# Performance work log

Hardware: AMD Instinct MI355X
Metric: run time of the kernel (lower is better)

The kernel has to match this reference:

```python
import jax, jax.numpy as jnp
import numpy as np

B, T, F, M = 32, 256, 512, 4   # batch, pred_len (=d_model=state_size), feature_dim (=mamba seq), time-mark feats
N = F - M                      # number of variates in x_enc
T2 = 2 * T
EPS = 1e-5


def setup_inputs() -> dict:
    key = jax.random.key(0)
    it = iter(jax.random.split(key, 32))
    def nrm(*s):
        return jax.random.normal(next(it), s, jnp.float32) * 0.02
    inp = {
        "x_enc": jax.random.normal(next(it), (B, T, N), jnp.float32),
        "x_mark_enc": jax.random.normal(next(it), (B, T, M), jnp.float32),
        "x_dec": jnp.zeros((1, 1, 1), jnp.float32),
        "x_mark_dec": jnp.zeros((1, 1, 1), jnp.float32),
        # 3 structurally identical MambaBlocks -> stack params on leading dim 3
        "norm_w": jnp.ones((3, T), jnp.float32),
        "inp_W": nrm(3, T, T2), "inp_b": jnp.zeros((3, T2), jnp.float32),
        "conv_W": nrm(3, F, F, 3), "conv_b": jnp.zeros((3, F), jnp.float32),
        "convlin_W": nrm(3, T2, T2), "convlin_b": jnp.zeros((3, T2), jnp.float32),
        "fc1_W": nrm(3, T2, T2), "fc1_b": jnp.zeros((3, T2), jnp.float32),
        "fc2_W": nrm(3, T2, T), "fc2_b": jnp.zeros((3, T), jnp.float32),
        "fc3_W": nrm(3, T2, T), "fc3_b": jnp.zeros((3, T), jnp.float32),
        "D_W": nrm(3, T, T2), "D_b": jnp.zeros((3, T2), jnp.float32),
        "out_W": nrm(3, T2, T), "out_b": jnp.ones((3, T), jnp.float32),  # out_proj.bias init to 1.0
        "proj_W": nrm(T, T), "proj_b": jnp.zeros((T,), jnp.float32),
    }
    return inp


def _rmsnorm(x, w):
    return x * jax.lax.rsqrt(jnp.mean(x * x, -1, keepdims=True) + EPS) * w


def _conv1d(x, W, b):
    # x: [B, C, L], W: [C_out, C_in, 3], padding=1
    y = jax.lax.conv_general_dilated(x, W, (1,), [(1, 1)], dimension_numbers=("NCH", "OIH", "NCH"))
    return y + b[None, :, None]


def _s6(x, fc1W, fc1b, fc2W, fc2b, fc3W, fc3b):
    # h is zero-initialized each call, so dA=exp(delta*A) multiplies zeros and
    # y = einsum('bln,bldn->bld', C, x[...,None]*dB) = delta * x * <C,B>_n
    Bmat = x @ fc2W + fc2b                         # [B, L, n]
    Cmat = x @ fc3W + fc3b                         # [B, L, n]
    delta = jax.nn.softplus(x @ fc1W + fc1b)       # [B, L, d]
    cb = jnp.einsum("bln,bln->bl", Cmat, Bmat)   # contraction over state dim
    return delta * x * cb[:, :, None]


def _block(x, i, p):
    xn = _rmsnorm(x, p["norm_w"][i])
    xp = xn @ p["inp_W"][i] + p["inp_b"][i]                      # [B, F, 2T]
    xc = jax.nn.silu(_conv1d(xp, p["conv_W"][i], p["conv_b"][i]))
    xco = xc @ p["convlin_W"][i] + p["convlin_b"][i]
    xssm = _s6(xco, p["fc1_W"][i], p["fc1_b"][i], p["fc2_W"][i], p["fc2_b"][i], p["fc3_W"][i], p["fc3_b"][i])
    xres = jax.nn.silu(xn @ p["D_W"][i] + p["D_b"][i])
    return (jax.nn.silu(xssm) * xres) @ p["out_W"][i] + p["out_b"][i]


def _forward(x_enc, x_mark_enc, p):
    means = jax.lax.stop_gradient(jnp.mean(x_enc, 1, keepdims=True))  # detached in torch
    xe = x_enc - means
    stdev = jnp.sqrt(jnp.var(xe, axis=1, keepdims=True) + 1e-5)       # NOT detached in torch
    xe = xe / stdev
    x = jnp.concatenate([xe, x_mark_enc], axis=2).transpose(0, 2, 1)  # [B, F, T]
    for i in range(3):
        x = _block(x, i, p)
    dec = (x @ p["proj_W"] + p["proj_b"]).transpose(0, 2, 1)          # [B, T, F]
    return dec[:, :, :N] * stdev + means                              # pred_len == T


def reference(x_enc, x_mark_enc, x_dec, x_mark_dec, norm_w, inp_W, inp_b, conv_W, conv_b, convlin_W, convlin_b, fc1_W, fc1_b, fc2_W, fc2_b, fc3_W, fc3_b, D_W, D_b, out_W, out_b, proj_W, proj_b):
    p = dict(norm_w=norm_w, inp_W=inp_W, inp_b=inp_b, conv_W=conv_W, conv_b=conv_b, convlin_W=convlin_W, convlin_b=convlin_b, fc1_W=fc1_W, fc1_b=fc1_b, fc2_W=fc2_W, fc2_b=fc2_b, fc3_W=fc3_W, fc3_b=fc3_b, D_W=D_W, D_b=D_b, out_W=out_W, out_b=out_b, proj_W=proj_W, proj_b=proj_b)
    return _forward(x_enc, x_mark_enc, p)
```

## Files before the change

### kernel.cpp

```cpp
#include <hip/hip_runtime.h>
#include <hip/hip_bf16.h>
#include <math.h>

typedef __hip_bfloat16 bf16;
typedef short short8 __attribute__((ext_vector_type(8)));
typedef short short4v __attribute__((ext_vector_type(4)));
typedef float floatx4 __attribute__((ext_vector_type(4)));

constexpr int CB_ = 32;
constexpr int CT = 256;
constexpr int CF = 512;
constexpr int CN = 508;
constexpr int CM = 4;
constexpr int CT2 = 512;
constexpr int MROWS = CB_ * CF;
constexpr int PADL = 528;

__device__ __forceinline__ float b2f(bf16 v) { return __bfloat162float(v); }
__device__ __forceinline__ bf16 f2b(float v) { return __float2bfloat16(v); }
__device__ __forceinline__ float s2f(short s) {
    unsigned u = ((unsigned)(unsigned short)s) << 16;
    return __builtin_bit_cast(float, u);
}
__device__ __forceinline__ short f2s(float v) {
    bf16 t = __float2bfloat16(v);
    return __builtin_bit_cast(short, t);
}
__device__ __forceinline__ float silu_f(float x) { return x / (1.0f + __expf(-x)); }
__device__ __forceinline__ float softplus_f(float x) {
    return fmaxf(x, 0.0f) + __logf(1.0f + __expf(-fabsf(x)));
}

__device__ __forceinline__ void gl_lds16(const bf16* g, short* l) {
    __builtin_amdgcn_global_load_lds(
        (const __attribute__((address_space(1))) unsigned int*)(g),
        (__attribute__((address_space(3))) unsigned int*)(l), 16, 0, 0);
}

constexpr int CONVN = 3 * 3 * 512 * 512;
constexpr int MTILES = 3520;
struct P8 { const float* s[8]; bf16* d[8]; };
__global__ __launch_bounds__(256) void prepack_all_kernel(P8 p, const float* __restrict__ nw,
                                                          const float* __restrict__ convW,
                                                          bf16* __restrict__ convD,
                                                          bf16* __restrict__ xpT,
                                                          float* __restrict__ CBv) {
    int bid = blockIdx.x;
    if (bid >= MTILES) {
        int idx = (bid - MTILES) * 256 + threadIdx.x;
        if (idx < CONVN) {
            int ci = idx & 511;
            int co = (idx >> 9) & 511;
            int it = idx >> 18;
            int tap = it % 3, ib = it / 3;
            convD[idx] = f2b(convW[(((size_t)(ib * 512 + co)) * 512 + ci) * 3 + tap]);
        } else if (idx < CONVN + 32768) {
            int j = idx - CONVN;
            int ci = j & 511;
            int w = (j >> 9) & 1;
            int b = j >> 10;
            xpT[((size_t)b * PADL + (w ? 513 : 0)) * 512 + ci] = f2b(0.0f);
        } else if (idx < CONVN + 32768 + MROWS) {
            CBv[idx - CONVN - 32768] = 0.0f;
        }
        return;
    }
    const int Ks[8]   = {256, 256, 512, 512, 512, 512, 512, 256};
    const int Ns[8]   = {512, 512, 512, 256, 256, 512, 256, 256};
    const int zs[8]   = {3, 3, 3, 3, 3, 3, 3, 1};
    const int dstr[8] = {262144, 262144, 524288, 524288, 524288, 262144, 131072, 65536};
    const int rml[8]  = {1, 1, 1, 2, 2, 1, 1, 1};
    const int rad[8]  = {0, 0, 0, 0, 1, 0, 0, 0};
    int m = 0, acc = 0;
    for (m = 0; m < 8; m++) {
        int c = (Ns[m] >> 5) * (Ks[m] >> 5) * zs[m];
        if (bid < acc + c) break;
        acc += c;
    }
    int lid = bid - acc;
    int K = Ks[m], N = Ns[m];
    int tx = N >> 5, ty = K >> 5;
    int z = lid / (tx * ty), rem = lid % (tx * ty);
    int k0 = (rem / tx) * 32, n0 = (rem % tx) * 32;
    const float* s = p.s[m] + (size_t)z * K * N;
    bf16* d = p.d[m] + (size_t)z * dstr[m];
    int mul = rml[m], add = rad[m];
    bool fold = (m <= 1);
    __shared__ float Ts[32][33];
    for (int e = threadIdx.x; e < 1024; e += 256) {
        int r = e >> 5, c = e & 31;
        float v = s[(size_t)(k0 + r) * N + n0 + c];
        if (fold) v *= nw[z * 256 + k0 + r];
        Ts[r][c] = v;
    }
    __syncthreads();
    for (int e = threadIdx.x; e < 1024; e += 256) {
        int r = e >> 5, c = e & 31;
        d[(size_t)((n0 + r) * mul + add) * K + k0 + c] = f2b(Ts[c][r]);
    }
}

__global__ __launch_bounds__(256) void buildx_kernel(
    const float* __restrict__ xe, const float* __restrict__ xm,
    float* __restrict__ means, float* __restrict__ stdev,
    bf16* __restrict__ X0, float* __restrict__ SCL) {
    __shared__ float L[256][65];
    __shared__ float red_s[4][64], red_q[4][64];
    __shared__ float stat_m[64], stat_i[64];
    int blk = blockIdx.x;
    int b = blk >> 3, f0 = (blk & 7) * 64;
    int tid = threadIdx.x;
    int j = tid & 63, tq = tid >> 6;
    int f = f0 + j;
    float ps = 0.f, pq = 0.f;
    const float* xep = xe + (size_t)b * CT * CN + f;
    const float* xmp = xm + (size_t)b * CT * CM + (f - CN);
    #pragma unroll 4
    for (int tt = 0; tt < 64; tt++) {
        int t = tq * 64 + tt;
        float v = (f < CN) ? xep[(size_t)t * CN] : xmp[(size_t)t * CM];
        L[t][j] = v;
        ps += v;
        pq += v * v;
    }
    red_s[tq][j] = ps;
    red_q[tq][j] = pq;
    __syncthreads();
    if (tid < 64) {
        int ff = f0 + tid;
        float s = red_s[0][tid] + red_s[1][tid] + red_s[2][tid] + red_s[3][tid];
        float q = red_q[0][tid] + red_q[1][tid] + red_q[2][tid] + red_q[3][tid];
        float mean, isd, msq;
        if (ff < CN) {
            mean = s * (1.0f / 256.0f);
            float var = fmaxf(q * (1.0f / 256.0f) - mean * mean, 0.0f);
            float sd = sqrtf(var + 1e-5f);
            isd = 1.0f / sd;
            means[b * CN + ff] = mean;
            stdev[b * CN + ff] = sd;
            msq = var / (var + 1e-5f);
        } else {
            mean = 0.0f;
            isd = 1.0f;
            msq = q * (1.0f / 256.0f);
        }
        stat_m[tid] = mean;
        stat_i[tid] = isd;
        SCL[b * 512 + ff] = rsqrtf(msq + 1e-5f);
    }
    __syncthreads();
    bf16* outp = X0 + ((size_t)(b * 512 + f0)) * 256;
    int t = tid;
    #pragma unroll 4
    for (int fp = 0; fp < 64; fp++) {
        float val = (L[t][fp] - stat_m[fp]) * stat_i[fp];
        outp[(size_t)fp * 256 + t] = f2b(val);
    }
}

template <int MODE>
__global__ __launch_bounds__(256) void mgemm_kernel(const bf16* __restrict__ A,
                                                    const bf16* __restrict__ Wt,
                                                    const float* __restrict__ b1,
                                                    const float* __restrict__ b2,
                                                    const float* __restrict__ SCL,
                                                    bf16* __restrict__ o1,
                                                    bf16* __restrict__ o2,
                                                    int K, int Ncols) {
    __shared__ __align__(16) short As[128 * 32];
    __shared__ __align__(16) short Bs[128 * 32];
    const int tid = threadIdx.x;
    const int lane = tid & 63;
    const int wave = tid >> 6;
    const int m0 = blockIdx.x * 128, n0 = blockIdx.y * 128;

    const int srow0 = wave * 32;
    const int lrow = lane >> 2;
    const int lcol = (lane & 3) * 8;

    const bf16* aP0 = A + (size_t)(m0 + srow0 + lrow) * K + lcol;
    const bf16* aP1 = A + (size_t)(m0 + srow0 + 16 + lrow) * K + lcol;
    const bf16* bP0 = Wt + (size_t)(n0 + srow0 + lrow) * K + lcol;
    const bf16* bP1 = Wt + (size_t)(n0 + srow0 + 16 + lrow) * K + lcol;
    short* aL0 = &As[srow0 * 32];
    short* aL1 = &As[(srow0 + 16) * 32];
    short* bL0 = &Bs[srow0 * 32];
    short* bL1 = &Bs[(srow0 + 16) * 32];

    const int wm = (wave & 1) * 64, wn = (wave >> 1) * 64;
    const int fr = lane & 15, quad = lane >> 4;

    floatx4 acc[4][4];
    #pragma unroll
    for (int i = 0; i < 4; i++)
        #pragma unroll
        for (int j = 0; j < 4; j++) acc[i][j] = (floatx4){0.f, 0.f, 0.f, 0.f};

    for (int k0 = 0; k0 < K; k0 += 32) {
        gl_lds16(aP0 + k0, aL0);
        gl_lds16(aP1 + k0, aL1);
        gl_lds16(bP0 + k0, bL0);
        gl_lds16(bP1 + k0, bL1);
        __syncthreads();
        short8 af[4], bfv[4];
        #pragma unroll
        for (int i = 0; i < 4; i++) af[i] = *(const short8*)&As[(wm + i * 16 + fr) * 32 + quad * 8];
        #pragma unroll
        for (int j = 0; j < 4; j++) bfv[j] = *(const short8*)&Bs[(wn + j * 16 + fr) * 32 + quad * 8];
        #pragma unroll
        for (int i = 0; i < 4; i++)
            #pragma unroll
            for (int j = 0; j < 4; j++)
                acc[i][j] = __builtin_amdgcn_mfma_f32_16x16x32_bf16(af[i], bfv[j], acc[i][j], 0, 0, 0);
        __syncthreads();
    }

    if (MODE == 0) {
        #pragma unroll
        for (int j = 0; j < 4; j++) {
            int n = n0 + wn + j * 16 + fr;
            float bv = b1[n];
            #pragma unroll
            for (int i = 0; i < 4; i++) {
                int mb = m0 + wm + i * 16 + quad * 4;
                #pragma unroll
                for (int r = 0; r < 4; r++)
                    o1[(size_t)(mb + r) * Ncols + n] = f2b(acc[i][j][r] + bv);
            }
        }
    } else {
        if (n0 + wn < 512) {
            int b = (m0 + wm) >> 9;
            #pragma unroll
            for (int i = 0; i < 4; i++) {
                int mb = m0 + wm + i * 16 + quad * 4;
                float sclr[4];
                #pragma unroll
                for (int r = 0; r < 4; r++) sclr[r] = SCL[mb + r];
                #pragma unroll
                for (int j = 0; j < 4; j++) {
                    int n = n0 + wn + j * 16 + fr;
                    float bv = b1[n];
                    bf16* dst = o1 + ((size_t)b * PADL + n + 1) * 512;
                    int ci = mb & 511;
                    short4v pk;
                    #pragma unroll
                    for (int r = 0; r < 4; r++) pk[r] = f2s(acc[i][j][r] * sclr[r] + bv);
                    *(short4v*)(dst + ci) = pk;
                }
            }
        } else {
            #pragma unroll
            for (int i = 0; i < 4; i++) {
                int mb = m0 + wm + i * 16 + quad * 4;
                float sclr[4];
                #pragma unroll
                for (int r = 0; r < 4; r++) sclr[r] = SCL[mb + r];
                #pragma unroll
                for (int j = 0; j < 4; j++) {
                    int n = n0 + wn + j * 16 + fr;
                    float bv = b2[n - 512];
                    #pragma unroll
                    for (int r = 0; r < 4; r++)
                        o2[(size_t)(mb + r) * 512 + (n - 512)] =
                            f2b(silu_f(acc[i][j][r] * sclr[r] + bv));
                }
            }
        }
    }
}

__global__ __launch_bounds__(256) void cbgemm_kernel(const bf16* __restrict__ A,
                                                     const bf16* __restrict__ Wt,
                                                     const float* __restrict__ b2,
                                                     const float* __restrict__ b3,
                                                     float* __restrict__ CBv) {
    __shared__ __align__(16) short As[128 * 32];
    __shared__ __align__(16) short Bs[128 * 32];
    const int tid = threadIdx.x;
    const int lane = tid & 63;
    const int wave = tid >> 6;
    const int m0 = blockIdx.x * 128, n0 = blockIdx.y * 128;

    const int srow0 = wave * 32;
    const int lrow = lane >> 2;
    const int lcol = (lane & 3) * 8;
    const bf16* aP0 = A + (size_t)(m0 + srow0 + lrow) * 512 + lcol;
    const bf16* aP1 = A + (size_t)(m0 + srow0 + 16 + lrow) * 512 + lcol;
    const bf16* bP0 = Wt + (size_t)(n0 + srow0 + lrow) * 512 + lcol;
    const bf16* bP1 = Wt + (size_t)(n0 + srow0 + 16 + lrow) * 512 + lcol;
    short* aL0 = &As[srow0 * 32];
    short* aL1 = &As[(srow0 + 16) * 32];
    short* bL0 = &Bs[srow0 * 32];
    short* bL1 = &Bs[(srow0 + 16) * 32];

    const int wm = (wave & 1) * 64, wn = (wave >> 1) * 64;
    const int fr = lane & 15, quad = lane >> 4;

    floatx4 acc[4][4];
    #pragma unroll
    for (int i = 0; i < 4; i++)
        #pragma unroll
        for (int j = 0; j < 4; j++) acc[i][j] = (floatx4){0.f, 0.f, 0.f, 0.f};

    for (int k0 = 0; k0 < 512; k0 += 32) {
        gl_lds16(aP0 + k0, aL0);
        gl_lds16(aP1 + k0, aL1);
        gl_lds16(bP0 + k0, bL0);
        gl_lds16(bP1 + k0, bL1);
        __syncthreads();
        short8 af[4], bfv[4];
        #pragma unroll
        for (int i = 0; i < 4; i++) af[i] = *(const short8*)&As[(wm + i * 16 + fr) * 32 + quad * 8];
        #pragma unroll
        for (int j = 0; j < 4; j++) bfv[j] = *(const short8*)&Bs[(wn + j * 16 + fr) * 32 + quad * 8];
        #pragma unroll
        for (int i = 0; i < 4; i++)
            #pragma unroll
            for (int j = 0; j < 4; j++)
                acc[i][j] = __builtin_amdgcn_mfma_f32_16x16x32_bf16(af[i], bfv[j], acc[i][j], 0, 0, 0);
        __syncthreads();
    }
    int nnb = n0 + wn;
    float bv[4];
    #pragma unroll
    for (int j = 0; j < 4; j++) {
        int nn = nnb + j * 16 + fr;
        int c = nn >> 1;
        bv[j] = (fr & 1) ? b3[c] : b2[c];
    }
    #pragma unroll
    for (int i = 0; i < 4; i++) {
        #pragma unroll
        for (int r = 0; r < 4; r++) {
            float s = 0.f;
            #pragma unroll
            for (int j = 0; j < 4; j++) {
                float v = acc[i][j][r] + bv[j];
                s += v * __shfl_xor(v, 1);
            }
            s += __shfl_xor(s, 2);
            s += __shfl_xor(s, 4);
            s += __shfl_xor(s, 8);
            if (fr == 0)
                atomicAdd(&CBv[m0 + wm + i * 16 + quad * 4 + r], s * 0.5f);
        }
    }
}

__global__ __launch_bounds__(256) void fc1gate_kernel(const bf16* __restrict__ A,
                                                      const bf16* __restrict__ Wt,
                                                      const float* __restrict__ b1,
                                                      const float* __restrict__ CBv,
                                                      const bf16* __restrict__ Xres,
                                                      bf16* __restrict__ G) {
    __shared__ __align__(16) short As[128 * 32];
    __shared__ __align__(16) short Bs[128 * 32];
    const int tid = threadIdx.x;
    const int lane = tid & 63;
    const int wave = tid >> 6;
    const int m0 = blockIdx.x * 128, n0 = blockIdx.y * 128;

    const int srow0 = wave * 32;
    const int lrow = lane >> 2;
    const int lcol = (lane & 3) * 8;
    const bf16* aP0 = A + (size_t)(m0 + srow0 + lrow) * 512 + lcol;
    const bf16* aP1 = A + (size_t)(m0 + srow0 + 16 + lrow) * 512 + lcol;
    const bf16* bP0 = Wt + (size_t)(n0 + srow0 + lrow) * 512 + lcol;
    const bf16* bP1 = Wt + (size_t)(n0 + srow0 + 16 + lrow) * 512 + lcol;
    short* aL0 = &As[srow0 * 32];
    short* aL1 = &As[(srow0 + 16) * 32];
    short* bL0 = &Bs[srow0 * 32];
    short* bL1 = &Bs[(srow0 + 16) * 32];

    const int wm = (wave & 1) * 64, wn = (wave >> 1) * 64;
    const int fr = lane & 15, quad = lane >> 4;

    floatx4 acc[4][4];
    #pragma unroll
    for (int i = 0; i < 4; i++)
        #pragma unroll
        for (int j = 0; j < 4; j++) acc[i][j] = (floatx4){0.f, 0.f, 0.f, 0.f};

    for (int k0 = 0; k0 < 512; k0 += 32) {
        gl_lds16(aP0 + k0, aL0);
        gl_lds16(aP1 + k0, aL1);
        gl_lds16(bP0 + k0, bL0);
        gl_lds16(bP1 + k0, bL1);
        __syncthreads();
        short8 af[4], bfv[4];
        #pragma unroll
        for (int i = 0; i < 4; i++) af[i] = *(const short8*)&As[(wm + i * 16 + fr) * 32 + quad * 8];
        #pragma unroll
        for (int j = 0; j < 4; j++) bfv[j] = *(const short8*)&Bs[(wn + j * 16 + fr) * 32 + quad * 8];
        #pragma unroll
        for (int i = 0; i < 4; i++)
            #pragma unroll
            for (int j = 0; j < 4; j++)
                acc[i][j] = __builtin_amdgcn_mfma_f32_16x16x32_bf16(af[i], bfv[j], acc[i][j], 0, 0, 0);
        __syncthreads();
    }
    #pragma unroll
    for (int i = 0; i < 4; i++) {
        int mb = m0 + wm + i * 16 + quad * 4;
        float cbr[4];
        #pragma unroll
        for (int r = 0; r < 4; r++) cbr[r] = CBv[mb + r];
        #pragma unroll
        for (int j = 0; j < 4; j++) {
            int n = n0 + wn + j * 16 + fr;
            float bv = b1[n];
            #pragma unroll
            for (int r = 0; r < 4; r++) {
                size_t off = (size_t)(mb + r) * 512 + n;
                float delta = softplus_f(acc[i][j][r] + bv);
                float xssm = delta * b2f(A[off]) * cbr[r];
                G[off] = f2b(silu_f(xssm) * b2f(Xres[off]));
            }
        }
    }
}

__global__ __launch_bounds__(256) void conv_mfma_kernel(const bf16* __restrict__ Wc,
                                                        const bf16* __restrict__ xpT,
                                                        const float* __restrict__ bias,
                                                        bf16* __restrict__ Out,
                                                        float* __restrict__ CBvZ) {
    __shared__ __align__(16) short As[3 * 128 * 32];
    __shared__ __align__(16) short Bs[144 * 32];
    const int tid = threadIdx.x;
    const int lane = tid & 63;
    const int wave = tid >> 6;
    int bx = blockIdx.x;
    if (bx < 128 && tid < 128) CBvZ[bx * 128 + tid] = 0.0f;
    int xcd = bx & 7, g = bx >> 3;
    int mt = g & 3;
    int id = xcd * 16 + (g >> 2);
    int nt = id & 3, b = id >> 2;
    const int m0 = mt * 128, n0 = nt * 128;
    const bf16* xb = xpT + (size_t)b * PADL * 512;

    const int lrow = lane >> 2;
    const int lcol = (lane & 3) * 8;
    const int wm = (wave & 1) * 64, wn = (wave >> 1) * 64;
    const int fr = lane & 15, quad = lane >> 4;

    floatx4 acc[4][4];
    #pragma unroll
    for (int i = 0; i < 4; i++)
        #pragma unroll
        for (int j = 0; j < 4; j++) acc[i][j] = (floatx4){0.f, 0.f, 0.f, 0.f};

    for (int k0 = 0; k0 < 512; k0 += 32) {
        for (int ga = wave; ga < 24; ga += 4) {
            int tap = ga >> 3, rg = ga & 7;
            gl_lds16(Wc + (size_t)tap * 262144 + (size_t)(m0 + rg * 16 + lrow) * 512 + k0 + lcol,
                     &As[ga * 512]);
        }
        for (int gb = wave; gb < 9; gb += 4) {
            gl_lds16(xb + (size_t)(n0 + gb * 16 + lrow) * 512 + k0 + lcol, &Bs[gb * 512]);
        }
        __syncthreads();
        #pragma unroll
        for (int tap = 0; tap < 3; tap++) {
            short8 af[4], bfv[4];
            #pragma unroll
            for (int i = 0; i < 4; i++)
                af[i] = *(const short8*)&As[tap * 4096 + (wm + i * 16 + fr) * 32 + quad * 8];
            #pragma unroll
            for (int j = 0; j < 4; j++)
                bfv[j] = *(const short8*)&Bs[(wn + j * 16 + fr + tap) * 32 + quad * 8];
            #pragma unroll
            for (int i = 0; i < 4; i++)
                #pragma unroll
                for (int j = 0; j < 4; j++)
                    acc[i][j] = __builtin_amdgcn_mfma_f32_16x16x32_bf16(af[i], bfv[j], acc[i][j], 0, 0, 0);
        }
        __syncthreads();
    }
    bf16* ob = Out + (size_t)b * CF * CT2;
    #pragma unroll
    for (int i = 0; i < 4; i++) {
        int mb = m0 + wm + i * 16 + quad * 4;
        #pragma unroll
        for (int r = 0; r < 4; r++) {
            float bv = bias[mb + r];
            #pragma unroll
            for (int j = 0; j < 4; j++) {
                int n = n0 + wn + j * 16 + fr;
                ob[(size_t)(mb + r) * CT2 + n] = f2b(silu_f(acc[i][j][r] + bv));
            }
        }
    }
}

__global__ __launch_bounds__(256) void gemm_scl_kernel(const bf16* __restrict__ A,
                                                       const bf16* __restrict__ Wt,
                                                       const float* __restrict__ bias,
                                                       bf16* __restrict__ Xo,
                                                       float* __restrict__ SCL) {
    __shared__ __align__(16) short As[64 * 32];
    __shared__ __align__(16) short Bs[256 * 32];
    __shared__ float red[4][64];
    const int tid = threadIdx.x;
    const int lane = tid & 63;
    const int wave = tid >> 6;
    const int m0 = blockIdx.x * 64;

    const int lrow = lane >> 2;
    const int lcol = (lane & 3) * 8;
    const bf16* aP = A + (size_t)(m0 + wave * 16 + lrow) * 512 + lcol;
    short* aL = &As[wave * 16 * 32];
    const bf16* bP[4];
    short* bL[4];
    #pragma unroll
    for (int g = 0; g < 4; g++) {
        int r0 = (wave * 4 + g) * 16;
        bP[g] = Wt + (size_t)(r0 + lrow) * 512 + lcol;
        bL[g] = &Bs[r0 * 32];
    }
    const int wn = wave * 64;
    const int fr = lane & 15, quad = lane >> 4;

    floatx4 acc[4][4];
    #pragma unroll
    for (int i = 0; i < 4; i++)
        #pragma unroll
        for (int j = 0; j < 4; j++) acc[i][j] = (floatx4){0.f, 0.f, 0.f, 0.f};

    for (int k0 = 0; k0 < 512; k0 += 32) {
        gl_lds16(aP + k0, aL);
        #pragma unroll
        for (int g = 0; g < 4; g++) gl_lds16(bP[g] + k0, bL[g]);
        __syncthreads();
        short8 af[4], bfv[4];
        #pragma unroll
        for (int i = 0; i < 4; i++) af[i] = *(const short8*)&As[(i * 16 + fr) * 32 + quad * 8];
        #pragma unroll
        for (int j = 0; j < 4; j++) bfv[j] = *(const short8*)&Bs[(wn + j * 16 + fr) * 32 + quad * 8];
        #pragma unroll
        for (int i = 0; i < 4; i++)
            #pragma unroll
            for (int j = 0; j < 4; j++)
                acc[i][j] = __builtin_amdgcn_mfma_f32_16x16x32_bf16(af[i], bfv[j], acc[i][j], 0, 0, 0);
        __syncthreads();
    }
    #pragma unroll
    for (int j = 0; j < 4; j++) {
        float bv = bias[wn + j * 16 + fr];
        #pragma unroll
        for (int i = 0; i < 4; i++)
            #pragma unroll
            for (int r = 0; r < 4; r++) acc[i][j][r] += bv;
    }
    #pragma unroll
    for (int i = 0; i < 4; i++) {
        #pragma unroll
        for (int r = 0; r < 4; r++) {
            float s = 0.f;
            #pragma unroll
            for (int j = 0; j < 4; j++) s += acc[i][j][r] * acc[i][j][r];
            #pragma unroll
            for (int o = 8; o > 0; o >>= 1) s += __shfl_xor(s, o);
            if (fr == 0) red[wave][i * 16 + quad * 4 + r] = s;
        }
    }
    __syncthreads();
    if (tid < 64) {
        float tot = red[0][tid] + red[1][tid] + red[2][tid] + red[3][tid];
        SCL[m0 + tid] = rsqrtf(tot * (1.0f / CT) + 1e-5f);
    }
    #pragma unroll
    for (int j = 0; j < 4; j++) {
        int n = wn + j * 16 + fr;
        #pragma unroll
        for (int i = 0; i < 4; i++) {
            int rl = i * 16 + quad * 4;
            #pragma unroll
            for (int r = 0; r < 4; r++)
                Xo[(size_t)(m0 + rl + r) * CT + n] = f2b(acc[i][j][r]);
        }
    }
}

__global__ __launch_bounds__(256) void proj_out_kernel(const bf16* __restrict__ A,
                                                       const bf16* __restrict__ Wt,
                                                       const float* __restrict__ bias,
                                                       const float* __restrict__ means,
                                                       const float* __restrict__ stdev,
                                                       float* __restrict__ out) {
    __shared__ __align__(16) short As[128 * 32];
    __shared__ __align__(16) short Bs[128 * 32];
    const int tid = threadIdx.x;
    const int lane = tid & 63;
    const int wave = tid >> 6;
    const int m0 = blockIdx.x * 128, n0 = blockIdx.y * 128;

    const int srow0 = wave * 32;
    const int lrow = lane >> 2;
    const int lcol = (lane & 3) * 8;
    const bf16* aP0 = A + (size_t)(m0 + srow0 + lrow) * 256 + lcol;
    const bf16* aP1 = A + (size_t)(m0 + srow0 + 16 + lrow) * 256 + lcol;
    const bf16* bP0 = Wt + (size_t)(n0 + srow0 + lrow) * 256 + lcol;
    const bf16* bP1 = Wt + (size_t)(n0 + srow0 + 16 + lrow) * 256 + lcol;
    short* aL0 = &As[srow0 * 32];
    short* aL1 = &As[(srow0 + 16) * 32];
    short* bL0 = &Bs[srow0 * 32];
    short* bL1 = &Bs[(srow0 + 16) * 32];

    const int wm = (wave & 1) * 64, wn = (wave >> 1) * 64;
    const int fr = lane & 15, quad = lane >> 4;

    floatx4 acc[4][4];
    #pragma unroll
    for (int i = 0; i < 4; i++)
        #pragma unroll
        for (int j = 0; j < 4; j++) acc[i][j] = (floatx4){0.f, 0.f, 0.f, 0.f};

    for (int k0 = 0; k0 < 256; k0 += 32) {
        gl_lds16(aP0 + k0, aL0);
        gl_lds16(aP1 + k0, aL1);
        gl_lds16(bP0 + k0, bL0);
        gl_lds16(bP1 + k0, bL1);
        __syncthreads();
        short8 af[4], bfv[4];
        #pragma unroll
        for (int i = 0; i < 4; i++) af[i] = *(const short8*)&As[(wm + i * 16 + fr) * 32 + quad * 8];
        #pragma unroll
        for (int j = 0; j < 4; j++) bfv[j] = *(const short8*)&Bs[(wn + j * 16 + fr) * 32 + quad * 8];
        #pragma unroll
        for (int i = 0; i < 4; i++)
            #pragma unroll
            for (int j = 0; j < 4; j++)
                acc[i][j] = __builtin_amdgcn_mfma_f32_16x16x32_bf16(af[i], bfv[j], acc[i][j], 0, 0, 0);
        __syncthreads();
    }
    #pragma unroll
    for (int j = 0; j < 4; j++) {
        int t = n0 + wn + j * 16 + fr;
        float bv = bias[t];
        #pragma unroll
        for (int i = 0; i < 4; i++) {
            int mb = m0 + wm + i * 16 + quad * 4;
            int b = mb >> 9;
            int nv = mb & 511;
            if (nv < CN) {
                floatx4 o;
                #pragma unroll
                for (int r = 0; r < 4; r++) {
                    int sn = b * CN + nv + r;
                    o[r] = (acc[i][j][r] + bv) * stdev[sn] + means[sn];
                }
                *(floatx4*)(out + ((size_t)(b * CT + t)) * CN + nv) = o;
            }
        }
    }
}

extern "C" void kernel_launch(void* const* d_in, const int* in_sizes, int n_in,
                              void* d_out, int out_size, void* d_ws, size_t ws_size,
                              hipStream_t stream) {
    const float* x_enc  = (const float*)d_in[0];
    const float* x_mark = (const float*)d_in[1];
    const float* norm_w = (const float*)d_in[4];
    const float* inp_W  = (const float*)d_in[5];
    const float* inp_b  = (const float*)d_in[6];
    const float* conv_W = (const float*)d_in[7];
    const float* conv_b = (const float*)d_in[8];
    const float* convlin_W = (const float*)d_in[9];
    const float* convlin_b = (const float*)d_in[10];
    const float* fc1_W = (const float*)d_in[11];
    const float* fc1_b = (const float*)d_in[12];
    const float* fc2_W = (const float*)d_in[13];
    const float* fc2_b = (const float*)d_in[14];
    const float* fc3_W = (const float*)d_in[15];
    const float* fc3_b = (const float*)d_in[16];
    const float* D_W   = (const float*)d_in[17];
    const float* D_b   = (const float*)d_in[18];
    const float* out_W = (const float*)d_in[19];
    const float* out_b = (const float*)d_in[20];
    const float* proj_W = (const float*)d_in[21];
    const float* proj_b = (const float*)d_in[22];

    char* ws = (char*)d_ws;
    float* MEANS = (float*)(ws);
    float* STDEV = (float*)(ws + 65536);
    float* CBv   = (float*)(ws + 131072);
    float* SCL   = (float*)(ws + 196608);
    bf16* wt = (bf16*)(ws + 262144);
    bf16* wt_g1      = wt;
    bf16* wt_g3      = wt + 786432;
    bf16* wt_convlin = wt + 2359296;
    bf16* wt_out     = wt + 3145728;
    bf16* wt_proj    = wt + 3538944;
    bf16* wt_conv    = wt + 3604480;
    bf16* xpT = (bf16*)(ws + 12189696);
    const size_t POOLB = 16777216;
    bf16* pool[4] = {
        (bf16*)(ws + 29491200),
        (bf16*)(ws + 29491200 + POOLB),
        (bf16*)(ws + 29491200 + 2 * POOLB),
        (bf16*)(ws + 29491200 + 3 * POOLB),
    };
    float* out = (float*)d_out;

    P8 p;
    p.s[0] = inp_W;  p.d[0] = wt_g1;
    p.s[1] = D_W;    p.d[1] = wt_g1 + 131072;
    p.s[2] = fc1_W;  p.d[2] = wt_g3;
    p.s[3] = fc2_W;  p.d[3] = wt_g3 + 262144;
    p.s[4] = fc3_W;  p.d[4] = wt_g3 + 262144;
    p.s[5] = convlin_W; p.d[5] = wt_convlin;
    p.s[6] = out_W;  p.d[6] = wt_out;
    p.s[7] = proj_W; p.d[7] = wt_proj;
    int convBlocks = (CONVN + 32768 + MROWS + 255) / 256;
    prepack_all_kernel<<<MTILES + convBlocks, 256, 0, stream>>>(
        p, norm_w, conv_W, wt_conv, xpT, CBv);

    buildx_kernel<<<256, 256, 0, stream>>>(x_enc, x_mark, MEANS, STDEV, pool[0], SCL);

    int ia = 0, ico = 1, ires = 2, iout = 3;
    for (int i = 0; i < 3; i++) {
        bf16* A  = pool[ia];
        bf16* XCO = pool[ico];
        bf16* XRES = pool[ires];
        bf16* OUTP = pool[iout];

        mgemm_kernel<1><<<dim3(128, 8), 256, 0, stream>>>(
            A, wt_g1 + (size_t)i * 262144, inp_b + i * CT2, D_b + i * CT2, SCL,
            xpT, XRES, 256, 1024);
        conv_mfma_kernel<<<512, 256, 0, stream>>>(wt_conv + (size_t)i * 786432, xpT,
                                                  conv_b + i * CF, A, CBv);
        mgemm_kernel<0><<<dim3(128, 4), 256, 0, stream>>>(
            A, wt_convlin + (size_t)i * 262144, convlin_b + i * CT2, nullptr, nullptr,
            XCO, nullptr, 512, 512);
        cbgemm_kernel<<<dim3(128, 4), 256, 0, stream>>>(
            XCO, wt_g3 + (size_t)i * 524288 + 262144, fc2_b + i * CT, fc3_b + i * CT, CBv);
        fc1gate_kernel<<<dim3(128, 4), 256, 0, stream>>>(
            XCO, wt_g3 + (size_t)i * 524288, fc1_b + i * CT2, CBv, XRES, A);
        gemm_scl_kernel<<<256, 256, 0, stream>>>(
            A, wt_out + (size_t)i * 131072, out_b + i * CT, OUTP, SCL);

        int na = iout, nco = ia, nres = ico, nout = ires;
        ia = na; ico = nco; ires = nres; iout = nout;
    }

    proj_out_kernel<<<dim3(128, 2), 256, 0, stream>>>(
        pool[ia], wt_proj, proj_b, MEANS, STDEV, out);
}
```

Before: 558.7 us.

## Double K-tile depth to 64 with XOR-swizzled LDS layout in all GEMMs

Every MFMA GEMM kernel now stages a K-slice of 64 instead of 32 per iteration, which halves the number of barrier pairs and global-to-LDS load rounds. LDS rows are 128 bytes wide and use an XOR swizzle on the 16-byte column chunk, so the fragment reads avoid bank conflicts. The conv kernel's shifted-row reads use a swizzle that accounts for the tap offset. The cost is double the LDS footprint per block, which may lower occupancy, most of all in the conv kernel.

```diff
diff --git a/kernel.cpp b/kernel.cpp
--- a/kernel.cpp
+++ b/kernel.cpp
@@ -18,10 +18,6 @@
 
 __device__ __forceinline__ float b2f(bf16 v) { return __bfloat162float(v); }
 __device__ __forceinline__ bf16 f2b(float v) { return __float2bfloat16(v); }
-__device__ __forceinline__ float s2f(short s) {
-    unsigned u = ((unsigned)(unsigned short)s) << 16;
-    return __builtin_bit_cast(float, u);
-}
 __device__ __forceinline__ short f2s(float v) {
     bf16 t = __float2bfloat16(v);
     return __builtin_bit_cast(short, t);
@@ -36,6 +32,7 @@
         (const __attribute__((address_space(1))) unsigned int*)(g),
         (__attribute__((address_space(3))) unsigned int*)(l), 16, 0, 0);
 }
+
 
 constexpr int CONVN = 3 * 3 * 512 * 512;
 constexpr int MTILES = 3520;
@@ -167,28 +164,32 @@
                                                     bf16* __restrict__ o1,
                                                     bf16* __restrict__ o2,
                                                     int K, int Ncols) {
-    __shared__ __align__(16) short As[128 * 32];
-    __shared__ __align__(16) short Bs[128 * 32];
+    __shared__ __align__(16) short As[128 * 64];
+    __shared__ __align__(16) short Bs[128 * 64];
     const int tid = threadIdx.x;
     const int lane = tid & 63;
     const int wave = tid >> 6;
     const int m0 = blockIdx.x * 128, n0 = blockIdx.y * 128;
 
     const int srow0 = wave * 32;
-    const int lrow = lane >> 2;
-    const int lcol = (lane & 3) * 8;
-
-    const bf16* aP0 = A + (size_t)(m0 + srow0 + lrow) * K + lcol;
-    const bf16* aP1 = A + (size_t)(m0 + srow0 + 16 + lrow) * K + lcol;
-    const bf16* bP0 = Wt + (size_t)(n0 + srow0 + lrow) * K + lcol;
-    const bf16* bP1 = Wt + (size_t)(n0 + srow0 + 16 + lrow) * K + lcol;
-    short* aL0 = &As[srow0 * 32];
-    short* aL1 = &As[(srow0 + 16) * 32];
-    short* bL0 = &Bs[srow0 * 32];
-    short* bL1 = &Bs[(srow0 + 16) * 32];
+    const int lrow8 = lane >> 3;
+    const int lcolS = (((lane & 7) ^ lrow8) << 3);
+
+    const bf16* aPc[4];
+    const bf16* bPc[4];
+    short* aLc[4];
+    short* bLc[4];
+    #pragma unroll
+    for (int c = 0; c < 4; c++) {
+        aPc[c] = A + (size_t)(m0 + srow0 + c * 8 + lrow8) * K + lcolS;
+        bPc[c] = Wt + (size_t)(n0 + srow0 + c * 8 + lrow8) * K + lcolS;
+        aLc[c] = &As[(srow0 + c * 8) * 64];
+        bLc[c] = &Bs[(srow0 + c * 8) * 64];
+    }
 
     const int wm = (wave & 1) * 64, wn = (wave >> 1) * 64;
     const int fr = lane & 15, quad = lane >> 4;
+    const int fr7 = fr & 7;
 
     floatx4 acc[4][4];
     #pragma unroll
@@ -196,22 +197,27 @@
         #pragma unroll
         for (int j = 0; j < 4; j++) acc[i][j] = (floatx4){0.f, 0.f, 0.f, 0.f};
 
-    for (int k0 = 0; k0 < K; k0 += 32) {
-        gl_lds16(aP0 + k0, aL0);
-        gl_lds16(aP1 + k0, aL1);
-        gl_lds16(bP0 + k0, bL0);
-        gl_lds16(bP1 + k0, bL1);
-        __syncthreads();
-        short8 af[4], bfv[4];
-        #pragma unroll
-        for (int i = 0; i < 4; i++) af[i] = *(const short8*)&As[(wm + i * 16 + fr) * 32 + quad * 8];
-        #pragma unroll
-        for (int j = 0; j < 4; j++) bfv[j] = *(const short8*)&Bs[(wn + j * 16 + fr) * 32 + quad * 8];
-        #pragma unroll
-        for (int i = 0; i < 4; i++)
-            #pragma unroll
-            for (int j = 0; j < 4; j++)
-                acc[i][j] = __builtin_amdgcn_mfma_f32_16x16x32_bf16(af[i], bfv[j], acc[i][j], 0, 0, 0);
+    for (int k0 = 0; k0 < K; k0 += 64) {
+        #pragma unroll
+        for (int c = 0; c < 4; c++) {
+            gl_lds16(aPc[c] + k0, aLc[c]);
+            gl_lds16(bPc[c] + k0, bLc[c]);
+        }
+        __syncthreads();
+        #pragma unroll
+        for (int s = 0; s < 2; s++) {
+            const int co = (((s * 4 + quad) ^ fr7) << 3);
+            short8 af[4], bfv[4];
+            #pragma unroll
+            for (int i = 0; i < 4; i++) af[i] = *(const short8*)&As[(wm + i * 16 + fr) * 64 + co];
+            #pragma unroll
+            for (int j = 0; j < 4; j++) bfv[j] = *(const short8*)&Bs[(wn + j * 16 + fr) * 64 + co];
+            #pragma unroll
+            for (int i = 0; i < 4; i++)
+                #pragma unroll
+                for (int j = 0; j < 4; j++)
+                    acc[i][j] = __builtin_amdgcn_mfma_f32_16x16x32_bf16(af[i], bfv[j], acc[i][j], 0, 0, 0);
+        }
         __syncthreads();
     }
 
@@ -275,27 +281,31 @@
                                                      const float* __restrict__ b2,
                                                      const float* __restrict__ b3,
                                                      float* __restrict__ CBv) {
-    __shared__ __align__(16) short As[128 * 32];
-    __shared__ __align__(16) short Bs[128 * 32];
+    __shared__ __align__(16) short As[128 * 64];
+    __shared__ __align__(16) short Bs[128 * 64];
     const int tid = threadIdx.x;
     const int lane = tid & 63;
     const int wave = tid >> 6;
     const int m0 = blockIdx.x * 128, n0 = blockIdx.y * 128;
 
     const int srow0 = wave * 32;
-    const int lrow = lane >> 2;
-    const int lcol = (lane & 3) * 8;
-    const bf16* aP0 = A + (size_t)(m0 + srow0 + lrow) * 512 + lcol;
-    const bf16* aP1 = A + (size_t)(m0 + srow0 + 16 + lrow) * 512 + lcol;
-    const bf16* bP0 = Wt + (size_t)(n0 + srow0 + lrow) * 512 + lcol;
-    const bf16* bP1 = Wt + (size_t)(n0 + srow0 + 16 + lrow) * 512 + lcol;
-    short* aL0 = &As[srow0 * 32];
-    short* aL1 = &As[(srow0 + 16) * 32];
-    short* bL0 = &Bs[srow0 * 32];
-    short* bL1 = &Bs[(srow0 + 16) * 32];
+    const int lrow8 = lane >> 3;
+    const int lcolS = (((lane & 7) ^ lrow8) << 3);
+    const bf16* aPc[4];
+    const bf16* bPc[4];
+    short* aLc[4];
+    short* bLc[4];
+    #pragma unroll
+    for (int c = 0; c < 4; c++) {
+        aPc[c] = A + (size_t)(m0 + srow0 + c * 8 + lrow8) * 512 + lcolS;
+        bPc[c] = Wt + (size_t)(n0 + srow0 + c * 8 + lrow8) * 512 + lcolS;
+        aLc[c] = &As[(srow0 + c * 8) * 64];
+        bLc[c] = &Bs[(srow0 + c * 8) * 64];
+    }
 
     const int wm = (wave & 1) * 64, wn = (wave >> 1) * 64;
     const int fr = lane & 15, quad = lane >> 4;
+    const int fr7 = fr & 7;
 
     floatx4 acc[4][4];
     #pragma unroll
@@ -303,22 +313,27 @@
         #pragma unroll
         for (int j = 0; j < 4; j++) acc[i][j] = (floatx4){0.f, 0.f, 0.f, 0.f};
 
-    for (int k0 = 0; k0 < 512; k0 += 32) {
-        gl_lds16(aP0 + k0, aL0);
-        gl_lds16(aP1 + k0, aL1);
-        gl_lds16(bP0 + k0, bL0);
-        gl_lds16(bP1 + k0, bL1);
-        __syncthreads();
-        short8 af[4], bfv[4];
-        #pragma unroll
-        for (int i = 0; i < 4; i++) af[i] = *(const short8*)&As[(wm + i * 16 + fr) * 32 + quad * 8];
-        #pragma unroll
-        for (int j = 0; j < 4; j++) bfv[j] = *(const short8*)&Bs[(wn + j * 16 + fr) * 32 + quad * 8];
-        #pragma unroll
-        for (int i = 0; i < 4; i++)
-            #pragma unroll
-            for (int j = 0; j < 4; j++)
-                acc[i][j] = __builtin_amdgcn_mfma_f32_16x16x32_bf16(af[i], bfv[j], acc[i][j], 0, 0, 0);
+    for (int k0 = 0; k0 < 512; k0 += 64) {
+        #pragma unroll
+        for (int c = 0; c < 4; c++) {
+            gl_lds16(aPc[c] + k0, aLc[c]);
+            gl_lds16(bPc[c] + k0, bLc[c]);
+        }
+        __syncthreads();
+        #pragma unroll
+        for (int s = 0; s < 2; s++) {
+            const int co = (((s * 4 + quad) ^ fr7) << 3);
+            short8 af[4], bfv[4];
+            #pragma unroll
+            for (int i = 0; i < 4; i++) af[i] = *(const short8*)&As[(wm + i * 16 + fr) * 64 + co];
+            #pragma unroll
+            for (int j = 0; j < 4; j++) bfv[j] = *(const short8*)&Bs[(wn + j * 16 + fr) * 64 + co];
+            #pragma unroll
+            for (int i = 0; i < 4; i++)
+                #pragma unroll
+                for (int j = 0; j < 4; j++)
+                    acc[i][j] = __builtin_amdgcn_mfma_f32_16x16x32_bf16(af[i], bfv[j], acc[i][j], 0, 0, 0);
+        }
         __syncthreads();
     }
     int nnb = n0 + wn;
@@ -354,27 +369,31 @@
                                                       const float* __restrict__ CBv,
                                                       const bf16* __restrict__ Xres,
                                                       bf16* __restrict__ G) {
-    __shared__ __align__(16) short As[128 * 32];
-    __shared__ __align__(16) short Bs[128 * 32];
+    __shared__ __align__(16) short As[128 * 64];
+    __shared__ __align__(16) short Bs[128 * 64];
     const int tid = threadIdx.x;
     const int lane = tid & 63;
     const int wave = tid >> 6;
     const int m0 = blockIdx.x * 128, n0 = blockIdx.y * 128;
 
     const int srow0 = wave * 32;
-    const int lrow = lane >> 2;
-    const int lcol = (lane & 3) * 8;
-    const bf16* aP0 = A + (size_t)(m0 + srow0 + lrow) * 512 + lcol;
-    const bf16* aP1 = A + (size_t)(m0 + srow0 + 16 + lrow) * 512 + lcol;
-    const bf16* bP0 = Wt + (size_t)(n0 + srow0 + lrow) * 512 + lcol;
-    const bf16* bP1 = Wt + (size_t)(n0 + srow0 + 16 + lrow) * 512 + lcol;
-    short* aL0 = &As[srow0 * 32];
-    short* aL1 = &As[(srow0 + 16) * 32];
-    short* bL0 = &Bs[srow0 * 32];
-    short* bL1 = &Bs[(srow0 + 16) * 32];
+    const int lrow8 = lane >> 3;
+    const int lcolS = (((lane & 7) ^ lrow8) << 3);
+    const bf16* aPc[4];
+    const bf16* bPc[4];
+    short* aLc[4];
+    short* bLc[4];
+    #pragma unroll
+    for (int c = 0; c < 4; c++) {
+        aPc[c] = A + (size_t)(m0 + srow0 + c * 8 + lrow8) * 512 + lcolS;
+        bPc[c] = Wt + (size_t)(n0 + srow0 + c * 8 + lrow8) * 512 + lcolS;
+        aLc[c] = &As[(srow0 + c * 8) * 64];
+        bLc[c] = &Bs[(srow0 + c * 8) * 64];
+    }
 
     const int wm = (wave & 1) * 64, wn = (wave >> 1) * 64;
     const int fr = lane & 15, quad = lane >> 4;
+    const int fr7 = fr & 7;
 
     floatx4 acc[4][4];
     #pragma unroll
@@ -382,22 +401,27 @@
         #pragma unroll
         for (int j = 0; j < 4; j++) acc[i][j] = (floatx4){0.f, 0.f, 0.f, 0.f};
 
-    for (int k0 = 0; k0 < 512; k0 += 32) {
-        gl_lds16(aP0 + k0, aL0);
-        gl_lds16(aP1 + k0, aL1);
-        gl_lds16(bP0 + k0, bL0);
-        gl_lds16(bP1 + k0, bL1);
-        __syncthreads();
-        short8 af[4], bfv[4];
-        #pragma unroll
-        for (int i = 0; i < 4; i++) af[i] = *(const short8*)&As[(wm + i * 16 + fr) * 32 + quad * 8];
-        #pragma unroll
-        for (int j = 0; j < 4; j++) bfv[j] = *(const short8*)&Bs[(wn + j * 16 + fr) * 32 + quad * 8];
-        #pragma unroll
-        for (int i = 0; i < 4; i++)
-            #pragma unroll
-            for (int j = 0; j < 4; j++)
-                acc[i][j] = __builtin_amdgcn_mfma_f32_16x16x32_bf16(af[i], bfv[j], acc[i][j], 0, 0, 0);
+    for (int k0 = 0; k0 < 512; k0 += 64) {
+        #pragma unroll
+        for (int c = 0; c < 4; c++) {
+            gl_lds16(aPc[c] + k0, aLc[c]);
+            gl_lds16(bPc[c] + k0, bLc[c]);
+        }
+        __syncthreads();
+        #pragma unroll
+        for (int s = 0; s < 2; s++) {
+            const int co = (((s * 4 + quad) ^ fr7) << 3);
+            short8 af[4], bfv[4];
+            #pragma unroll
+            for (int i = 0; i < 4; i++) af[i] = *(const short8*)&As[(wm + i * 16 + fr) * 64 + co];
+            #pragma unroll
+            for (int j = 0; j < 4; j++) bfv[j] = *(const short8*)&Bs[(wn + j * 16 + fr) * 64 + co];
+            #pragma unroll
+            for (int i = 0; i < 4; i++)
+                #pragma unroll
+                for (int j = 0; j < 4; j++)
+                    acc[i][j] = __builtin_amdgcn_mfma_f32_16x16x32_bf16(af[i], bfv[j], acc[i][j], 0, 0, 0);
+        }
         __syncthreads();
     }
     #pragma unroll
@@ -426,8 +450,8 @@
                                                         const float* __restrict__ bias,
                                                         bf16* __restrict__ Out,
                                                         float* __restrict__ CBvZ) {
-    __shared__ __align__(16) short As[3 * 128 * 32];
-    __shared__ __align__(16) short Bs[144 * 32];
+    __shared__ __align__(16) short As[3 * 128 * 64];
+    __shared__ __align__(16) short Bs[144 * 64];
     const int tid = threadIdx.x;
     const int lane = tid & 63;
     const int wave = tid >> 6;
@@ -440,10 +464,11 @@
     const int m0 = mt * 128, n0 = nt * 128;
     const bf16* xb = xpT + (size_t)b * PADL * 512;
 
-    const int lrow = lane >> 2;
-    const int lcol = (lane & 3) * 8;
+    const int lrow8 = lane >> 3;
+    const int lcolS = (((lane & 7) ^ lrow8) << 3);
     const int wm = (wave & 1) * 64, wn = (wave >> 1) * 64;
     const int fr = lane & 15, quad = lane >> 4;
+    const int fr7 = fr & 7;
 
     floatx4 acc[4][4];
     #pragma unroll
@@ -451,30 +476,36 @@
         #pragma unroll
         for (int j = 0; j < 4; j++) acc[i][j] = (floatx4){0.f, 0.f, 0.f, 0.f};
 
-    for (int k0 = 0; k0 < 512; k0 += 32) {
-        for (int ga = wave; ga < 24; ga += 4) {
-            int tap = ga >> 3, rg = ga & 7;
-            gl_lds16(Wc + (size_t)tap * 262144 + (size_t)(m0 + rg * 16 + lrow) * 512 + k0 + lcol,
-                     &As[ga * 512]);
-        }
-        for (int gb = wave; gb < 9; gb += 4) {
-            gl_lds16(xb + (size_t)(n0 + gb * 16 + lrow) * 512 + k0 + lcol, &Bs[gb * 512]);
-        }
-        __syncthreads();
-        #pragma unroll
-        for (int tap = 0; tap < 3; tap++) {
-            short8 af[4], bfv[4];
-            #pragma unroll
-            for (int i = 0; i < 4; i++)
-                af[i] = *(const short8*)&As[tap * 4096 + (wm + i * 16 + fr) * 32 + quad * 8];
-            #pragma unroll
-            for (int j = 0; j < 4; j++)
-                bfv[j] = *(const short8*)&Bs[(wn + j * 16 + fr + tap) * 32 + quad * 8];
-            #pragma unroll
-            for (int i = 0; i < 4; i++)
+    for (int k0 = 0; k0 < 512; k0 += 64) {
+        for (int ga = wave; ga < 48; ga += 4) {
+            int tap = ga >> 4, rg = ga & 15;
+            gl_lds16(Wc + (size_t)tap * 262144 + (size_t)(m0 + rg * 8 + lrow8) * 512 + k0 + lcolS,
+                     &As[tap * 8192 + rg * 512]);
+        }
+        for (int gb = wave; gb < 18; gb += 4) {
+            gl_lds16(xb + (size_t)(n0 + gb * 8 + lrow8) * 512 + k0 + lcolS, &Bs[gb * 512]);
+        }
+        __syncthreads();
+        #pragma unroll
+        for (int s = 0; s < 2; s++) {
+            const int sq = s * 4 + quad;
+            #pragma unroll
+            for (int tap = 0; tap < 3; tap++) {
+                const int coA = ((sq ^ fr7) << 3);
+                const int coB = ((sq ^ ((fr + tap) & 7)) << 3);
+                short8 af[4], bfv[4];
+                #pragma unroll
+                for (int i = 0; i < 4; i++)
+                    af[i] = *(const short8*)&As[tap * 8192 + (wm + i * 16 + fr) * 64 + coA];
                 #pragma unroll
                 for (int j = 0; j < 4; j++)
-                    acc[i][j] = __builtin_amdgcn_mfma_f32_16x16x32_bf16(af[i], bfv[j], acc[i][j], 0, 0, 0);
+                    bfv[j] = *(const short8*)&Bs[(wn + j * 16 + fr + tap) * 64 + coB];
+                #pragma unroll
+                for (int i = 0; i < 4; i++)
+                    #pragma unroll
+                    for (int j = 0; j < 4; j++)
+                        acc[i][j] = __builtin_amdgcn_mfma_f32_16x16x32_bf16(af[i], bfv[j], acc[i][j], 0, 0, 0);
+            }
         }
         __syncthreads();
     }
@@ -499,28 +530,19 @@
                                                        const float* __restrict__ bias,
                                                        bf16* __restrict__ Xo,
                                                        float* __restrict__ SCL) {
-    __shared__ __align__(16) short As[64 * 32];
-    __shared__ __align__(16) short Bs[256 * 32];
+    __shared__ __align__(16) short As[64 * 64];
+    __shared__ __align__(16) short Bs[256 * 64];
     __shared__ float red[4][64];
     const int tid = threadIdx.x;
     const int lane = tid & 63;
     const int wave = tid >> 6;
     const int m0 = blockIdx.x * 64;
 
-    const int lrow = lane >> 2;
-    const int lcol = (lane & 3) * 8;
-    const bf16* aP = A + (size_t)(m0 + wave * 16 + lrow) * 512 + lcol;
-    short* aL = &As[wave * 16 * 32];
-    const bf16* bP[4];
-    short* bL[4];
-    #pragma unroll
-    for (int g = 0; g < 4; g++) {
-        int r0 = (wave * 4 + g) * 16;
-        bP[g] = Wt + (size_t)(r0 + lrow) * 512 + lcol;
-        bL[g] = &Bs[r0 * 32];
-    }
+    const int lrow8 = lane >> 3;
+    const int lcolS = (((lane & 7) ^ lrow8) << 3);
     const int wn = wave * 64;
     const int fr = lane & 15, quad = lane >> 4;
+    const int fr7 = fr & 7;
 
     floatx4 acc[4][4];
     #pragma unroll
@@ -528,21 +550,26 @@
         #pragma unroll
         for (int j = 0; j < 4; j++) acc[i][j] = (floatx4){0.f, 0.f, 0.f, 0.f};
 
-    for (int k0 = 0; k0 < 512; k0 += 32) {
-        gl_lds16(aP + k0, aL);
-        #pragma unroll
-        for (int g = 0; g < 4; g++) gl_lds16(bP[g] + k0, bL[g]);
-        __syncthreads();
-        short8 af[4], bfv[4];
-        #pragma unroll
-        for (int i = 0; i < 4; i++) af[i] = *(const short8*)&As[(i * 16 + fr) * 32 + quad * 8];
-        #pragma unroll
-        for (int j = 0; j < 4; j++) bfv[j] = *(const short8*)&Bs[(wn + j * 16 + fr) * 32 + quad * 8];
-        #pragma unroll
-        for (int i = 0; i < 4; i++)
-            #pragma unroll
-            for (int j = 0; j < 4; j++)
-                acc[i][j] = __builtin_amdgcn_mfma_f32_16x16x32_bf16(af[i], bfv[j], acc[i][j], 0, 0, 0);
+    for (int k0 = 0; k0 < 512; k0 += 64) {
+        for (int c = wave; c < 8; c += 4)
+            gl_lds16(A + (size_t)(m0 + c * 8 + lrow8) * 512 + k0 + lcolS, &As[c * 512]);
+        for (int c = wave; c < 32; c += 4)
+            gl_lds16(Wt + (size_t)(c * 8 + lrow8) * 512 + k0 + lcolS, &Bs[c * 512]);
+        __syncthreads();
+        #pragma unroll
+        for (int s = 0; s < 2; s++) {
+            const int co = (((s * 4 + quad) ^ fr7) << 3);
+            short8 af[4], bfv[4];
+            #pragma unroll
+            for (int i = 0; i < 4; i++) af[i] = *(const short8*)&As[(i * 16 + fr) * 64 + co];
+            #pragma unroll
+            for (int j = 0; j < 4; j++) bfv[j] = *(const short8*)&Bs[(wn + j * 16 + fr) * 64 + co];
+            #pragma unroll
+            for (int i = 0; i < 4; i++)
+                #pragma unroll
+                for (int j = 0; j < 4; j++)
+                    acc[i][j] = __builtin_amdgcn_mfma_f32_16x16x32_bf16(af[i], bfv[j], acc[i][j], 0, 0, 0);
+        }
         __syncthreads();
     }
     #pragma unroll
@@ -589,27 +616,31 @@
                                                        const float* __restrict__ means,
                                                        const float* __restrict__ stdev,
                                                        float* __restrict__ out) {
-    __shared__ __align__(16) short As[128 * 32];
-    __shared__ __align__(16) short Bs[128 * 32];
+    __shared__ __align__(16) short As[128 * 64];
+    __shared__ __align__(16) short Bs[128 * 64];
     const int tid = threadIdx.x;
     const int lane = tid & 63;
     const int wave = tid >> 6;
     const int m0 = blockIdx.x * 128, n0 = blockIdx.y * 128;
 
     const int srow0 = wave * 32;
-    const int lrow = lane >> 2;
-    const int lcol = (lane & 3) * 8;
-    const bf16* aP0 = A + (size_t)(m0 + srow0 + lrow) * 256 + lcol;
-    const bf16* aP1 = A + (size_t)(m0 + srow0 + 16 + lrow) * 256 + lcol;
-    const bf16* bP0 = Wt + (size_t)(n0 + srow0 + lrow) * 256 + lcol;
-    const bf16* bP1 = Wt + (size_t)(n0 + srow0 + 16 + lrow) * 256 + lcol;
-    short* aL0 = &As[srow0 * 32];
-    short* aL1 = &As[(srow0 + 16) * 32];
-    short* bL0 = &Bs[srow0 * 32];
-    short* bL1 = &Bs[(srow0 + 16) * 32];
+    const int lrow8 = lane >> 3;
+    const int lcolS = (((lane & 7) ^ lrow8) << 3);
+    const bf16* aPc[4];
+    const bf16* bPc[4];
+    short* aLc[4];
+    short* bLc[4];
+    #pragma unroll
+    for (int c = 0; c < 4; c++) {
+        aPc[c] = A + (size_t)(m0 + srow0 + c * 8 + lrow8) * 256 + lcolS;
+        bPc[c] = Wt + (size_t)(n0 + srow0 + c * 8 + lrow8) * 256 + lcolS;
+        aLc[c] = &As[(srow0 + c * 8) * 64];
+        bLc[c] = &Bs[(srow0 + c * 8) * 64];
+    }
 
     const int wm = (wave & 1) * 64, wn = (wave >> 1) * 64;
     const int fr = lane & 15, quad = lane >> 4;
+    const int fr7 = fr & 7;
 
     floatx4 acc[4][4];
     #pragma unroll
@@ -617,22 +648,27 @@
         #pragma unroll
         for (int j = 0; j < 4; j++) acc[i][j] = (floatx4){0.f, 0.f, 0.f, 0.f};
 
-    for (int k0 = 0; k0 < 256; k0 += 32) {
-        gl_lds16(aP0 + k0, aL0);
-        gl_lds16(aP1 + k0, aL1);
-        gl_lds16(bP0 + k0, bL0);
-        gl_lds16(bP1 + k0, bL1);
-        __syncthreads();
-        short8 af[4], bfv[4];
-        #pragma unroll
-        for (int i = 0; i < 4; i++) af[i] = *(const short8*)&As[(wm + i * 16 + fr) * 32 + quad * 8];
-        #pragma unroll
-        for (int j = 0; j < 4; j++) bfv[j] = *(const short8*)&Bs[(wn + j * 16 + fr) * 32 + quad * 8];
-        #pragma unroll
-        for (int i = 0; i < 4; i++)
-            #pragma unroll
-            for (int j = 0; j < 4; j++)
-                acc[i][j] = __builtin_amdgcn_mfma_f32_16x16x32_bf16(af[i], bfv[j], acc[i][j], 0, 0, 0);
+    for (int k0 = 0; k0 < 256; k0 += 64) {
+        #pragma unroll
+        for (int c = 0; c < 4; c++) {
+            gl_lds16(aPc[c] + k0, aLc[c]);
+            gl_lds16(bPc[c] + k0, bLc[c]);
+        }
+        __syncthreads();
+        #pragma unroll
+        for (int s = 0; s < 2; s++) {
+            const int co = (((s * 4 + quad) ^ fr7) << 3);
+            short8 af[4], bfv[4];
+            #pragma unroll
+            for (int i = 0; i < 4; i++) af[i] = *(const short8*)&As[(wm + i * 16 + fr) * 64 + co];
+            #pragma unroll
+            for (int j = 0; j < 4; j++) bfv[j] = *(const short8*)&Bs[(wn + j * 16 + fr) * 64 + co];
+            #pragma unroll
+            for (int i = 0; i < 4; i++)
+                #pragma unroll
+                for (int j = 0; j < 4; j++)
+                    acc[i][j] = __builtin_amdgcn_mfma_f32_16x16x32_bf16(af[i], bfv[j], acc[i][j], 0, 0, 0);
+        }
         __syncthreads();
     }
     #pragma unroll
```

Measured after the change: 568.5 us. No clear change (+1.8%).
